# Kernel optimization log

Hardware: AMD Instinct MI355X
Metric: run time of the kernel (lower is better)

The kernel has to match this reference:

```python
import jax, jax.numpy as jnp
import numpy as np

B, N, CIN, C = 2, 400000, 192, 128
Y, X, Z = 512, 512, 40
EPS1 = 1e-5   # default BatchNorm1d eps for feature_proj
EPS2 = 1e-3   # norm_fn eps=0.001 for shared_conv BN


def setup_inputs() -> dict:
    key = jax.random.key(0)
    ks = jax.random.split(key, 12)
    voxel_features = jax.random.normal(ks[0], (N, CIN), jnp.float32)
    bi = jax.random.randint(ks[1], (N,), 0, B)
    zi = jax.random.randint(ks[2], (N,), 0, Z)
    yi = jax.random.randint(ks[3], (N,), 0, Y)
    xi = jax.random.randint(ks[4], (N,), 0, X)
    voxel_coords = jnp.stack([bi, zi, yi, xi], axis=1).astype(jnp.int32)  # (N,4)=[b,z,y,x]
    # feature_proj: Linear(CIN->C) + BN1d (inference stats) + ReLU
    W_proj = jax.random.normal(ks[5], (CIN, C), jnp.float32) * np.float32(1.0 / np.sqrt(CIN))
    b_proj = jnp.zeros((C,), jnp.float32)
    bn1_gamma = jnp.ones((C,), jnp.float32)
    bn1_beta = jnp.zeros((C,), jnp.float32)
    bn1_mean = jax.random.normal(ks[6], (C,), jnp.float32) * np.float32(0.1)
    bn1_var = jax.random.uniform(ks[7], (C,), jnp.float32, 0.5, 1.5)
    # shared_conv: SubMConv2d(C,C,3,pad=1,bias) + BN(eps=1e-3) + ReLU
    conv_w = jax.random.normal(ks[8], (3, 3, C, C), jnp.float32) * np.float32(1.0 / np.sqrt(9 * C))
    conv_b = jnp.zeros((C,), jnp.float32)
    bn2_gamma = jnp.ones((C,), jnp.float32)
    bn2_beta = jnp.zeros((C,), jnp.float32)
    bn2_mean = jax.random.normal(ks[9], (C,), jnp.float32) * np.float32(0.1)
    bn2_var = jax.random.uniform(ks[10], (C,), jnp.float32, 0.5, 1.5)
    return dict(voxel_features=voxel_features, voxel_coords=voxel_coords,
                W_proj=W_proj, b_proj=b_proj,
                bn1_gamma=bn1_gamma, bn1_beta=bn1_beta, bn1_mean=bn1_mean, bn1_var=bn1_var,
                conv_w=conv_w, conv_b=conv_b,
                bn2_gamma=bn2_gamma, bn2_beta=bn2_beta, bn2_mean=bn2_mean, bn2_var=bn2_var)


def reference(voxel_features, voxel_coords, W_proj, b_proj,
              bn1_gamma, bn1_beta, bn1_mean, bn1_var,
              conv_w, conv_b, bn2_gamma, bn2_beta, bn2_mean, bn2_var):
    # 1) feature_proj (Linear + BN1d inference + ReLU)
    f = voxel_features @ W_proj + b_proj                      # (N, C)
    f = (f - bn1_mean) * jax.lax.rsqrt(bn1_var + EPS1) * bn1_gamma + bn1_beta
    f = jax.nn.relu(f)
    # 2) bev_aggregate: unique([b,y,x]) + index_add == scatter-sum to dense BEV grid
    bi, yi, xi = voxel_coords[:, 0], voxel_coords[:, 2], voxel_coords[:, 3]
    dense = jnp.zeros((B, Y, X, C), f.dtype).at[bi, yi, xi].add(f)
    active = jnp.zeros((B, Y, X), bool).at[bi, yi, xi].set(True)
    # 3) SubMConv2d(3x3, pad=1) + BN + ReLU; subm == dense conv masked to active sites
    out = jax.lax.conv_general_dilated(dense, conv_w, (1, 1), 'SAME',
                                       dimension_numbers=('NHWC', 'HWIO', 'NHWC')) + conv_b
    out = (out - bn2_mean) * jax.lax.rsqrt(bn2_var + EPS2) * bn2_gamma + bn2_beta
    out = jax.nn.relu(out)
    # sparse tensor only holds active sites; zero elsewhere
    return jnp.where(active[..., None], out, jnp.float32(0.0))  # (B, Y, X, C)
```

## Files before the change

### kernel.cpp

```cpp
#include <hip/hip_runtime.h>

#define Bq 2
#define Yq 512
#define Xq 512
#define NVOX 400000

typedef __bf16 bf16x8 __attribute__((ext_vector_type(8)));
typedef float f32x4 __attribute__((ext_vector_type(4)));
typedef float f32x16 __attribute__((ext_vector_type(16)));
typedef short s16x8 __attribute__((ext_vector_type(8)));
typedef short s16x2 __attribute__((ext_vector_type(2)));

__device__ __forceinline__ short f2bf_s(float f){
    return __builtin_bit_cast(short, static_cast<__bf16>(f));
}

__device__ __forceinline__ void atomic_pk_add_bf16(short* addr, unsigned data){
#if __has_builtin(__builtin_amdgcn_global_atomic_fadd_v2bf16)
    s16x2 v; v[0] = (short)(data & 0xffff); v[1] = (short)(data >> 16);
    __builtin_amdgcn_global_atomic_fadd_v2bf16(
        (__attribute__((address_space(1))) s16x2*)addr, v);
#else
    asm volatile("global_atomic_pk_add_bf16 %0, %1, off"
                 :: "v"(addr), "v"(data) : "memory");
#endif
}

__global__ void kprep(const float* __restrict__ conv_w, const float* __restrict__ W_proj,
                      short* __restrict__ wTs, short* __restrict__ wpT){
    int tid = blockIdx.x*256 + threadIdx.x;
    if (tid < 9*128*128){
        int tap = tid >> 14; int r = tid & 16383; int co = r >> 7; int ci = r & 127;
        int g = ci >> 3, e = ci & 7;
        wTs[tap*16384 + co*128 + (((g & 8) | ((g & 7) ^ (co & 7))) << 3) + e] =
            f2bf_s(conv_w[tap*16384 + ci*128 + co]);
    }
    int e = tid - 9*128*128;
    if (e >= 0 && e < 128*192){
        int co = e / 192; int ci = e - co*192;
        wpT[e] = f2bf_s(W_proj[ci*128 + co]);
    }
}

__global__ void kcount(const int* __restrict__ vc, unsigned* __restrict__ cnt,
                       unsigned char* __restrict__ act){
    int i = blockIdx.x*256 + threadIdx.x;
    if (i >= NVOX) return;
    const int4 c = *reinterpret_cast<const int4*>(vc + i*4);
    int cell = (c.x*Yq + c.z)*Xq + c.w;
    act[cell] = 1;
    atomicAdd(&cnt[cell], 1u);
}

__global__ void __launch_bounds__(256, 2)
kproj(const float* __restrict__ vf, const int* __restrict__ vc,
      const unsigned* __restrict__ cnt,
      const short* __restrict__ wpT, const float* __restrict__ bp,
      const float* __restrict__ g1, const float* __restrict__ be1,
      const float* __restrict__ mu1, const float* __restrict__ va1,
      short* __restrict__ dbf){
    __shared__ short A[64*200];
    __shared__ int cellsPk[64];
    const int t = threadIdx.x;
    const int v0 = blockIdx.x * 64;

    const float4* vf4 = reinterpret_cast<const float4*>(vf);
    #pragma unroll
    for (int j = 0; j < 12; ++j){
        int i = t + j*256;
        int v = i / 48, kq = i - v*48;
        float4 x = vf4[(size_t)(v0 + v)*48 + kq];
        short4 s; s.x=f2bf_s(x.x); s.y=f2bf_s(x.y); s.z=f2bf_s(x.z); s.w=f2bf_s(x.w);
        *reinterpret_cast<short4*>(&A[v*200 + kq*4]) = s;
    }
    if (t < 64){
        int vi = v0 + t;
        int bi = vc[vi*4 + 0], yi = vc[vi*4 + 2], xi = vc[vi*4 + 3];
        unsigned cn = cnt[(bi*Yq + yi)*Xq + xi];
        int P = (bi*514 + (yi + 1))*514 + (xi + 1);
        cellsPk[t] = (P*8 + ((xi + 1) & 7)) | ((cn > 1) ? (1 << 30) : 0);
    }
    __syncthreads();

    const int w  = t >> 6;
    const int l  = t & 63;
    const int lr = l & 15;
    const int q  = l >> 4;

    const short* wp_lane = wpT + (size_t)(w*32 + lr)*192 + q*8;
    bf16x8 bb[2][6];
    #pragma unroll
    for (int n = 0; n < 2; ++n)
        #pragma unroll
        for (int kc = 0; kc < 6; ++kc)
            bb[n][kc] = *reinterpret_cast<const bf16x8*>(wp_lane + n*16*192 + kc*32);

    f32x4 acc[4][2] = {};
    #pragma unroll
    for (int kc = 0; kc < 6; ++kc){
        bf16x8 a[4];
        #pragma unroll
        for (int m = 0; m < 4; ++m)
            a[m] = *reinterpret_cast<const bf16x8*>(&A[(m*16 + lr)*200 + kc*32 + q*8]);
        #pragma unroll
        for (int m = 0; m < 4; ++m)
            #pragma unroll
            for (int n = 0; n < 2; ++n)
                acc[m][n] = __builtin_amdgcn_mfma_f32_16x16x32_bf16(a[m], bb[n][kc], acc[m][n], 0, 0, 0);
    }

    #pragma unroll
    for (int n = 0; n < 2; ++n){
        int c = w*32 + n*16 + lr;
        float s1  = g1[c] * rsqrtf(va1[c] + 1e-5f);
        float sh1 = be1[c] + (bp[c] - mu1[c]) * s1;
        #pragma unroll
        for (int m = 0; m < 4; ++m){
            #pragma unroll
            for (int r = 0; r < 4; ++r){
                int vx = m*16 + q*4 + r;
                float val = fmaxf(fmaf(acc[m][n][r], s1, sh1), 0.f);
                float vp  = __shfl_xor(val, 1);
                if ((lr & 1) == 0){
                    int pk = cellsPk[vx];
                    int multi = pk >> 30;
                    int P = (pk & 0x3fffffff) >> 3, xp7 = pk & 7;
                    short* addr = dbf + (size_t)P*128 + (((c >> 3) ^ xp7) << 3) + (c & 7);
                    unsigned data = (unsigned)(unsigned short)f2bf_s(val)
                                  | ((unsigned)(unsigned short)f2bf_s(vp) << 16);
                    if (!multi){
                        if (data) *reinterpret_cast<unsigned*>(addr) = data;
                    } else {
                        if (data) atomic_pk_add_bf16(addr, data);
                    }
                }
            }
        }
    }
}

__global__ void __launch_bounds__(512, 2)
kconv(const short* __restrict__ dbf, const short* __restrict__ wTs,
      const unsigned char* __restrict__ act, const float* __restrict__ cb,
      const float* __restrict__ g2, const float* __restrict__ be2,
      const float* __restrict__ mu2, const float* __restrict__ va2,
      float* __restrict__ out){
    __shared__ short Atile[6*1056*8];
    __shared__ short Bbuf[2][1024*8];
    const int t = threadIdx.x;
    const int bid = (blockIdx.x & 7)*256 + (blockIdx.x >> 3);
    const int b   = bid >> 10;
    const int rem = bid & 1023;
    const int y0  = (rem >> 3) << 2;
    const int x0  = (rem & 7) << 6;

    const int w   = t >> 6, l = t & 63;
    const int yy  = w >> 1, nn = w & 1;
    const int l31 = l & 31, hi = l >> 5;
    const int wbase16 = w*64*16;

    #define STAGE_B(BUF, H) do {                                              \
        const short* gb = wTs + (size_t)((H) >> 1)*16384 + ((H) & 1)*64;      \
        _Pragma("unroll")                                                     \
        for (int j = 0; j < 2; ++j){                                          \
            int S = j*512 + t;                                                \
            const short* gp = gb + (S >> 3)*128 + (S & 7)*8;                  \
            __builtin_amdgcn_global_load_lds(                                 \
                (const __attribute__((address_space(1))) void*)gp,            \
                (__attribute__((address_space(3))) void*)                    \
                    ((char*)Bbuf[BUF] + (size_t)(j*512*16) + wbase16), 16, 0, 0); \
        }                                                                     \
    } while(0)

    STAGE_B(0, 0);
    #pragma unroll
    for (int j = 0; j < 13; ++j){
        int S = j*512 + t;
        if (S < 6336){
            int r = S / 1056, s = S - r*1056;
            const short* gp = dbf + ((size_t)((b*514 + (y0 + r))*514 + x0)*16 + s)*8;
            __builtin_amdgcn_global_load_lds(
                (const __attribute__((address_space(1))) void*)gp,
                (__attribute__((address_space(3))) void*)
                    ((char*)Atile + (size_t)(j*512*16) + wbase16), 16, 0, 0);
        }
    }

    f32x16 acc[2][2] = {};
    const int bReadBase = (nn*64 + l31)*64;
    const int bXor = l31 & 7;

    #pragma unroll
    for (int h = 0; h < 18; ++h){
        asm volatile("s_waitcnt vmcnt(0)" ::: "memory");
        __builtin_amdgcn_s_barrier();
        __builtin_amdgcn_sched_barrier(0);
        if (h < 17) STAGE_B((h+1) & 1, h+1);
        const short* Bc = Bbuf[h & 1];
        const int tap = h >> 1, hh = h & 1;
        const int ky = tap / 3, kx = tap - ky*3;
        const int row = yy + ky;
        const int p0 = l31 + kx, p1 = p0 + 32;
        const int base0 = (row*1056 + p0*16)*8;
        const int base1 = (row*1056 + p1*16)*8;
        const int pk7 = p0 & 7;
        #pragma unroll
        for (int kc = 0; kc < 4; ++kc){
            const int ks  = kc*2 + hi;
            const int q   = ((hh*8 + ks) ^ pk7) << 3;
            const int qb  = (ks ^ bXor) << 3;
            bf16x8 a0 = *reinterpret_cast<const bf16x8*>(&Atile[base0 + q]);
            bf16x8 a1 = *reinterpret_cast<const bf16x8*>(&Atile[base1 + q]);
            bf16x8 b0 = *reinterpret_cast<const bf16x8*>(&Bc[bReadBase + qb]);
            bf16x8 b1 = *reinterpret_cast<const bf16x8*>(&Bc[bReadBase + 2048 + qb]);
            acc[0][0] = __builtin_amdgcn_mfma_f32_32x32x16_bf16(a0, b0, acc[0][0], 0, 0, 0);
            acc[0][1] = __builtin_amdgcn_mfma_f32_32x32x16_bf16(a0, b1, acc[0][1], 0, 0, 0);
            acc[1][0] = __builtin_amdgcn_mfma_f32_32x32x16_bf16(a1, b0, acc[1][0], 0, 0, 0);
            acc[1][1] = __builtin_amdgcn_mfma_f32_32x32x16_bf16(a1, b1, acc[1][1], 0, 0, 0);
        }
    }
    #undef STAGE_B

    const int yg = y0 + yy;
    const size_t rowcell = (size_t)(b*Yq + yg)*Xq + x0;
    #pragma unroll
    for (int ni = 0; ni < 2; ++ni){
        int c = nn*64 + ni*32 + l31;
        float s2  = g2[c] * rsqrtf(va2[c] + 1e-3f);
        float sh2 = be2[c] + (cb[c] - mu2[c]) * s2;
        #pragma unroll
        for (int mi = 0; mi < 2; ++mi){
            #pragma unroll
            for (int r = 0; r < 16; ++r){
                int pos = mi*32 + (r & 3) + ((r >> 2) << 3) + hi*4;
                size_t cell = rowcell + pos;
                float v = act[cell] ? fmaxf(fmaf(acc[mi][ni][r], s2, sh2), 0.f) : 0.f;
                out[cell*128 + c] = v;
            }
        }
    }
}

extern "C" void kernel_launch(void* const* d_in, const int* in_sizes, int n_in,
                              void* d_out, int out_size, void* d_ws, size_t ws_size,
                              hipStream_t stream){
    const float* vf  = (const float*)d_in[0];
    const int*   vc  = (const int*)  d_in[1];
    const float* Wp  = (const float*)d_in[2];
    const float* bp  = (const float*)d_in[3];
    const float* g1  = (const float*)d_in[4];
    const float* be1 = (const float*)d_in[5];
    const float* mu1 = (const float*)d_in[6];
    const float* va1 = (const float*)d_in[7];
    const float* cw  = (const float*)d_in[8];
    const float* cb  = (const float*)d_in[9];
    const float* g2  = (const float*)d_in[10];
    const float* be2 = (const float*)d_in[11];
    const float* mu2 = (const float*)d_in[12];
    const float* va2 = (const float*)d_in[13];
    float* out = (float*)d_out;
    char* ws = (char*)d_ws;

    if (ws_size < 138233856ull) return;
    short* dbf = (short*)ws;
    unsigned char* act = (unsigned char*)(ws + 135268352);
    short* wTs = (short*)(ws + 135792640);
    short* wpT = (short*)(ws + 136087552);
    unsigned* cnt = (unsigned*)(ws + 136136704);

    hipMemsetAsync(dbf, 0, 135268352, stream);
    hipMemsetAsync(act, 0, 524288, stream);
    hipMemsetAsync(cnt, 0, 2097152, stream);
    kprep<<<672, 256, 0, stream>>>(cw, Wp, wTs, wpT);
    kcount<<<1563, 256, 0, stream>>>(vc, cnt, act);
    kproj<<<6250, 256, 0, stream>>>(vf, vc, cnt, wpT, bp, g1, be1, mu1, va1, dbf);
    kconv<<<2048, 512, 0, stream>>>(dbf, wTs, act, cb, g2, be2, mu2, va2, out);
}
```

Before: 390.6 us.

## Stage projection scatter through LDS and deepen conv weight pipeline

In the projection kernel, each block's bf16 results are first written to shared memory and then stored to the dense grid with one wave per voxel. Each wave writes a full contiguous 256-byte row, replacing the strided 4-byte scatter from the MFMA layout. In the conv kernel, the weight buffer grows from 2 to 4 stages and is loaded two half-taps at a time, which halves the number of barriers. The A tile shrinks from 6 rows to 5, and the sixth row is loaded into slot 0 once row 0 is no longer needed, keeping LDS usage within budget. This adds ring-buffer reuse logic that must be timed correctly to avoid overwriting rows that are still being read.

```diff
diff --git a/kernel.cpp b/kernel.cpp
--- a/kernel.cpp
+++ b/kernel.cpp
@@ -59,8 +59,10 @@
       const float* __restrict__ g1, const float* __restrict__ be1,
       const float* __restrict__ mu1, const float* __restrict__ va1,
       short* __restrict__ dbf){
-    __shared__ short A[64*200];
+    __shared__ char smem[64*200*2];
     __shared__ int cellsPk[64];
+    short*    A  = (short*)smem;
+    unsigned* st = (unsigned*)smem;
     const int t = threadIdx.x;
     const int v0 = blockIdx.x * 64;
 
@@ -109,11 +111,14 @@
                 acc[m][n] = __builtin_amdgcn_mfma_f32_16x16x32_bf16(a[m], bb[n][kc], acc[m][n], 0, 0, 0);
     }
 
+    __syncthreads();
+    const int odd = lr & 1;
     #pragma unroll
     for (int n = 0; n < 2; ++n){
         int c = w*32 + n*16 + lr;
         float s1  = g1[c] * rsqrtf(va1[c] + 1e-5f);
         float sh1 = be1[c] + (bp[c] - mu1[c]) * s1;
+        int jj = w*16 + n*8 + (lr >> 1);
         #pragma unroll
         for (int m = 0; m < 4; ++m){
             #pragma unroll
@@ -121,20 +126,29 @@
                 int vx = m*16 + q*4 + r;
                 float val = fmaxf(fmaf(acc[m][n][r], s1, sh1), 0.f);
                 float vp  = __shfl_xor(val, 1);
-                if ((lr & 1) == 0){
-                    int pk = cellsPk[vx];
-                    int multi = pk >> 30;
-                    int P = (pk & 0x3fffffff) >> 3, xp7 = pk & 7;
-                    short* addr = dbf + (size_t)P*128 + (((c >> 3) ^ xp7) << 3) + (c & 7);
+                if (!odd){
                     unsigned data = (unsigned)(unsigned short)f2bf_s(val)
                                   | ((unsigned)(unsigned short)f2bf_s(vp) << 16);
-                    if (!multi){
-                        if (data) *reinterpret_cast<unsigned*>(addr) = data;
-                    } else {
-                        if (data) atomic_pk_add_bf16(addr, data);
-                    }
+                    st[vx*68 + jj] = data;
                 }
             }
+        }
+    }
+    __syncthreads();
+
+    unsigned* dbf_u32 = reinterpret_cast<unsigned*>(dbf);
+    #pragma unroll
+    for (int i = 0; i < 16; ++i){
+        int vv = w*16 + i;
+        int pk = cellsPk[vv];
+        int multi = pk >> 30;
+        int P = (pk & 0x3fffffff) >> 3, xp7 = pk & 7;
+        unsigned data = st[vv*68 + l];
+        size_t idx = (size_t)P*64 + (((l >> 2) ^ xp7) << 2) + (l & 3);
+        if (multi){
+            if (data) atomic_pk_add_bf16((short*)(dbf_u32 + idx), data);
+        } else {
+            dbf_u32[idx] = data;
         }
     }
 }
@@ -145,8 +159,8 @@
       const float* __restrict__ g2, const float* __restrict__ be2,
       const float* __restrict__ mu2, const float* __restrict__ va2,
       float* __restrict__ out){
-    __shared__ short Atile[6*1056*8];
-    __shared__ short Bbuf[2][1024*8];
+    __shared__ short Atile[5*1056*8];
+    __shared__ short Bbuf[4][1024*8];
     const int t = threadIdx.x;
     const int bid = (blockIdx.x & 7)*256 + (blockIdx.x >> 3);
     const int b   = bid >> 10;
@@ -173,10 +187,11 @@
     } while(0)
 
     STAGE_B(0, 0);
-    #pragma unroll
-    for (int j = 0; j < 13; ++j){
+    STAGE_B(1, 1);
+    #pragma unroll
+    for (int j = 0; j < 11; ++j){
         int S = j*512 + t;
-        if (S < 6336){
+        if (S < 5280){
             int r = S / 1056, s = S - r*1056;
             const short* gp = dbf + ((size_t)((b*514 + (y0 + r))*514 + x0)*16 + s)*8;
             __builtin_amdgcn_global_load_lds(
@@ -191,18 +206,37 @@
     const int bXor = l31 & 7;
 
     #pragma unroll
-    for (int h = 0; h < 18; ++h){
-        asm volatile("s_waitcnt vmcnt(0)" ::: "memory");
-        __builtin_amdgcn_s_barrier();
-        __builtin_amdgcn_sched_barrier(0);
-        if (h < 17) STAGE_B((h+1) & 1, h+1);
-        const short* Bc = Bbuf[h & 1];
-        const int tap = h >> 1, hh = h & 1;
+    for (int p = 0; p < 18; ++p){
+        if ((p & 1) == 0){
+            __builtin_amdgcn_sched_barrier(0);
+            asm volatile("s_waitcnt vmcnt(0)" ::: "memory");
+            __builtin_amdgcn_s_barrier();
+            __builtin_amdgcn_sched_barrier(0);
+            if (p + 2 < 18) STAGE_B((p+2) & 3, p+2);
+            if (p + 3 < 18) STAGE_B((p+3) & 3, p+3);
+            if (p == 6){
+                #pragma unroll
+                for (int j = 0; j < 3; ++j){
+                    int S = j*512 + t;
+                    if (S < 1056){
+                        const short* gp = dbf + ((size_t)((b*514 + (y0 + 5))*514 + x0)*16 + S)*8;
+                        __builtin_amdgcn_global_load_lds(
+                            (const __attribute__((address_space(1))) void*)gp,
+                            (__attribute__((address_space(3))) void*)
+                                ((char*)Atile + (size_t)(j*512 + w*64)*16), 16, 0, 0);
+                    }
+                }
+            }
+            __builtin_amdgcn_sched_barrier(0);
+        }
+        const short* Bc = Bbuf[p & 3];
+        const int tap = p >> 1, hh = p & 1;
         const int ky = tap / 3, kx = tap - ky*3;
         const int row = yy + ky;
+        const int rowp = (row >= 5) ? 0 : row;
         const int p0 = l31 + kx, p1 = p0 + 32;
-        const int base0 = (row*1056 + p0*16)*8;
-        const int base1 = (row*1056 + p1*16)*8;
+        const int base0 = (rowp*1056 + p0*16)*8;
+        const int base1 = (rowp*1056 + p1*16)*8;
         const int pk7 = p0 & 7;
         #pragma unroll
         for (int kc = 0; kc < 4; ++kc){
```

After: 358.5 us. -8.2%, faster.
